# Kernel optimization log

Measured on AMD Instinct MI355X. Metric: run time of the kernel, lower is better.

The kernel has to match this reference:

```python
import jax, jax.numpy as jnp
import numpy as np

NUM_NODES = 100000
NUM_EDGES = 6400000


def setup_inputs() -> dict:
    key = jax.random.key(0)
    k1, k2 = jax.random.split(key)
    e = jax.random.normal(k1, (NUM_EDGES,), dtype=jnp.float32)
    edge_index = jax.random.randint(k2, (2, NUM_EDGES), 0, NUM_NODES, dtype=jnp.int64 if jax.config.jax_enable_x64 else jnp.int32)
    return {"e": e, "edge_index": edge_index, "num_nodes": NUM_NODES}


def reference(e, edge_index, num_nodes):
    # GAT edge softmax (no max-subtraction, matching the 'simple' variant)
    target_nodes = edge_index[1]                      # [E]
    exp_e = jnp.exp(e)                                # [E]
    sum_exp = jax.ops.segment_sum(exp_e, target_nodes, num_segments=num_nodes)  # [N]
    alpha = exp_e / (sum_exp[target_nodes] + 1e-16)   # gather + normalize
    return alpha
```

## Files before the change

### kernel.cpp

```cpp
#include <hip/hip_runtime.h>


#define CHUNK 36864
#define SCAT_THREADS 1024
#define NPT 7
#define NSUB 8
#define ASSUMED_N 100000
#define SUMS_RESERVE (1u << 20)

__device__ __forceinline__ unsigned bf16rne(float f) {
    unsigned u = __float_as_uint(f);
    return (u + 0x7FFFu + ((u >> 16) & 1u)) >> 16;
}
__device__ __forceinline__ float bf16tof(unsigned short h) {
    return __uint_as_float(((unsigned)h) << 16);
}


__global__ __launch_bounds__(SCAT_THREADS, 4)
void gat_scatter_regcache(const float* __restrict__ e,
                          const int* __restrict__ tgt,
                          const int* __restrict__ np,
                          unsigned short* __restrict__ partials,
                          int per, int E, int Cmax) {
    __shared__ float hist[CHUNK];
    const int n = *np;
    int C = (n + CHUNK - 1) / CHUNK;
    if (C > Cmax) C = Cmax;

    const int b = blockIdx.x;
    const int tid = threadIdx.x;
    const long long start = (long long)b * per;

    int nv = per >> 2;
    long long rem = (long long)E - start;
    if (rem < 0) rem = 0;
    if ((long long)nv > (rem >> 2)) nv = (int)(rem >> 2);
    const int tail_lo = nv * 4;
    int tail_hi = per;
    if ((long long)tail_hi > rem) tail_hi = (int)rem;

    const float4* e4 = reinterpret_cast<const float4*>(e + start);
    const int4*  t4 = reinterpret_cast<const int4*>(tgt + start);

    float4 xv[NPT];
    int4   iv[NPT];
#pragma unroll
    for (int i = 0; i < NPT; ++i) {
        const int v = i * SCAT_THREADS + tid;
        if (v < nv) {
            const float4 ev = e4[v];
            iv[i] = t4[v];
            xv[i].x = __expf(ev.x); xv[i].y = __expf(ev.y);
            xv[i].z = __expf(ev.z); xv[i].w = __expf(ev.w);
        } else {
            iv[i].x = iv[i].y = iv[i].z = iv[i].w = -1;
            xv[i].x = xv[i].y = xv[i].z = xv[i].w = 0.0f;
        }
    }
#pragma unroll
    for (int i = 0; i < NPT; ++i) {
        asm volatile("" : "+v"(xv[i].x), "+v"(xv[i].y),
                          "+v"(xv[i].z), "+v"(xv[i].w),
                          "+v"(iv[i].x), "+v"(iv[i].y),
                          "+v"(iv[i].z), "+v"(iv[i].w));
    }

    for (int c = 0; c < C; ++c) {
        const int base = c * CHUNK;

        float4 z; z.x = z.y = z.z = z.w = 0.0f;
        for (int j = tid; j < (CHUNK / 4); j += SCAT_THREADS)
            reinterpret_cast<float4*>(hist)[j] = z;
        __syncthreads();

#pragma unroll
        for (int i = 0; i < NPT; ++i) {
            int t;
            t = iv[i].x - base; if ((unsigned)t < (unsigned)CHUNK) atomicAdd(&hist[t], xv[i].x);
            t = iv[i].y - base; if ((unsigned)t < (unsigned)CHUNK) atomicAdd(&hist[t], xv[i].y);
            t = iv[i].z - base; if ((unsigned)t < (unsigned)CHUNK) atomicAdd(&hist[t], xv[i].z);
            t = iv[i].w - base; if ((unsigned)t < (unsigned)CHUNK) atomicAdd(&hist[t], xv[i].w);
        }
        for (int i = tail_lo + tid; i < tail_hi; i += SCAT_THREADS) {
            int t = tgt[start + i] - base;
            if ((unsigned)t < (unsigned)CHUNK) atomicAdd(&hist[t], __expf(e[start + i]));
        }
        __syncthreads();

        unsigned* dst = reinterpret_cast<unsigned*>(
            partials + ((size_t)b * Cmax + c) * CHUNK);
        const float2* h2 = reinterpret_cast<const float2*>(hist);
        for (int j = tid; j < (CHUNK / 2); j += SCAT_THREADS) {
            const float2 hv = h2[j];
            dst[j] = bf16rne(hv.x) | (bf16rne(hv.y) << 16);
        }
        __syncthreads();
    }
}


__global__ void gat_reduce1(const unsigned short* __restrict__ partials,
                            float* __restrict__ subsums,
                            int B, int CC ) {
    const int nq = CC >> 2;
    const int t = blockIdx.x * blockDim.x + threadIdx.x;
    if (t >= nq * NSUB) return;
    const int s = t / nq;
    const int q = t - s * nq;
    const int nd = q * 4;
    const int bps = B / NSUB;
    const int b0 = s * bps;

    const unsigned short* p = partials + nd;
    float s0 = 0.f, s1 = 0.f, s2 = 0.f, s3 = 0.f;
    float r0 = 0.f, r1 = 0.f, r2 = 0.f, r3 = 0.f;
    for (int b = b0; b + 1 < b0 + bps; b += 2) {
        const ushort4 va = *reinterpret_cast<const ushort4*>(p + (size_t)b * CC);
        const ushort4 vb = *reinterpret_cast<const ushort4*>(p + (size_t)(b + 1) * CC);
        s0 += bf16tof(va.x); s1 += bf16tof(va.y);
        s2 += bf16tof(va.z); s3 += bf16tof(va.w);
        r0 += bf16tof(vb.x); r1 += bf16tof(vb.y);
        r2 += bf16tof(vb.z); r3 += bf16tof(vb.w);
    }
    float4 o;
    o.x = s0 + r0; o.y = s1 + r1; o.z = s2 + r2; o.w = s3 + r3;
    *reinterpret_cast<float4*>(subsums + (size_t)s * CC + nd) = o;
}


__global__ void gat_reduce2(const float* __restrict__ subsums,
                            const int* __restrict__ np,
                            float* __restrict__ sums,
                            int CC) {
    const int n = *np;
    const int q = blockIdx.x * blockDim.x + threadIdx.x;
    const int nd = q * 4;
    if (nd >= CC) return;
    float4 acc; acc.x = acc.y = acc.z = acc.w = 0.f;
#pragma unroll
    for (int s = 0; s < NSUB; ++s) {
        const float4 v = *reinterpret_cast<const float4*>(subsums + (size_t)s * CC + nd);
        acc.x += v.x; acc.y += v.y; acc.z += v.z; acc.w += v.w;
    }
    if (nd + 4 <= n) {
        *reinterpret_cast<float4*>(sums + nd) = acc;
    } else {
        if (nd     < n) sums[nd]     = acc.x;
        if (nd + 1 < n) sums[nd + 1] = acc.y;
        if (nd + 2 < n) sums[nd + 2] = acc.z;
        if (nd + 3 < n) sums[nd + 3] = acc.w;
    }
}


__global__ void gat_zero_sums(float* __restrict__ sums,
                              const int* __restrict__ np) {
    const int n = *np;
    const int stride = gridDim.x * blockDim.x;
    for (int i = blockIdx.x * blockDim.x + threadIdx.x; i < n; i += stride)
        sums[i] = 0.0f;
}

__global__ void gat_exp_scatter(const float4* __restrict__ e4,
                                const int4* __restrict__ t4,
                                const float* __restrict__ e,
                                const int* __restrict__ tgt,
                                float* __restrict__ sums,
                                int n4, int E) {
    const int stride = gridDim.x * blockDim.x;
    int tid = blockIdx.x * blockDim.x + threadIdx.x;
    for (int i = tid; i < n4; i += stride) {
        float4 ev = e4[i];
        int4 tv = t4[i];
        atomicAdd(&sums[tv.x], __expf(ev.x));
        atomicAdd(&sums[tv.y], __expf(ev.y));
        atomicAdd(&sums[tv.z], __expf(ev.z));
        atomicAdd(&sums[tv.w], __expf(ev.w));
    }
    const int tail_base = n4 * 4;
    const int tail_n = E - tail_base;
    if (tid < tail_n)
        atomicAdd(&sums[tgt[tail_base + tid]], __expf(e[tail_base + tid]));
}


__global__ void gat_normalize(const float4* __restrict__ e4,
                              const int4* __restrict__ t4,
                              const float* __restrict__ e,
                              const int* __restrict__ tgt,
                              const float* __restrict__ sums,
                              float4* __restrict__ out4,
                              float* __restrict__ out,
                              int n4, int E) {
    const int stride = gridDim.x * blockDim.x;
    int tid = blockIdx.x * blockDim.x + threadIdx.x;
    for (int i = tid; i < n4; i += stride) {
        float4 ev = e4[i];
        int4 tv = t4[i];
        float4 r;
        r.x = __expf(ev.x) * __builtin_amdgcn_rcpf(sums[tv.x] + 1e-16f);
        r.y = __expf(ev.y) * __builtin_amdgcn_rcpf(sums[tv.y] + 1e-16f);
        r.z = __expf(ev.z) * __builtin_amdgcn_rcpf(sums[tv.z] + 1e-16f);
        r.w = __expf(ev.w) * __builtin_amdgcn_rcpf(sums[tv.w] + 1e-16f);
        out4[i] = r;
    }
    const int tail_base = n4 * 4;
    const int tail_n = E - tail_base;
    if (tid < tail_n) {
        int i = tail_base + tid;
        out[i] = __expf(e[i]) * __builtin_amdgcn_rcpf(sums[tgt[i]] + 1e-16f);
    }
}

extern "C" void kernel_launch(void* const* d_in, const int* in_sizes, int n_in,
                              void* d_out, int out_size, void* d_ws, size_t ws_size,
                              hipStream_t stream) {
    const float* e = (const float*)d_in[0];
    const int* edge_index = (const int*)d_in[1];
    const int* num_nodes_p = (const int*)d_in[2];

    const int E = in_sizes[0];
    const int* tgt = edge_index + E;

    float* sums = (float*)d_ws;
    float* alpha = (float*)d_out;
    const int n4e = E / 4;

    const int Cmax = (ASSUMED_N + CHUNK - 1) / CHUNK;
    const int CC = Cmax * CHUNK;
    const int B = 256;
    const int per = (((E + B - 1) / B) + 3) & ~3;

    const size_t subs_off = SUMS_RESERVE;
    const size_t part_off = subs_off + (size_t)NSUB * CC * sizeof(float);

    bool use_chunked =
        (part_off + (size_t)B * CC * sizeof(unsigned short)) <= ws_size
        && per <= NPT * SCAT_THREADS * 4;

    if (use_chunked) {
        float* subsums = (float*)((char*)d_ws + subs_off);
        unsigned short* partials = (unsigned short*)((char*)d_ws + part_off);

        gat_scatter_regcache<<<B, SCAT_THREADS, 0, stream>>>(
            e, tgt, num_nodes_p, partials, per, E, Cmax);

        const int r1_threads = (CC / 4) * NSUB;
        gat_reduce1<<<(r1_threads + 255) / 256, 256, 0, stream>>>(
            partials, subsums, B, CC);

        gat_reduce2<<<(CC / 4 + 255) / 256, 256, 0, stream>>>(
            subsums, num_nodes_p, sums, CC);
    } else {
        gat_zero_sums<<<512, 256, 0, stream>>>(sums, num_nodes_p);
        int blocks = (n4e + 255) / 256;
        if (blocks > 2048) blocks = 2048;
        if (blocks < 1) blocks = 1;
        gat_exp_scatter<<<blocks, 256, 0, stream>>>(
            (const float4*)e, (const int4*)tgt, e, tgt, sums, n4e, E);
    }

    {
        int blocks = (n4e + 255) / 256;
        if (blocks < 1) blocks = 1;
        gat_normalize<<<blocks, 256, 0, stream>>>(
            (const float4*)e, (const int4*)tgt, e, tgt, sums,
            (float4*)alpha, alpha, n4e, E);
    }
}
```

Measured before the change: 95.74 us.

## Split node range across blocks instead of looping chunks with register-cached edges

The scatter kernel used to keep each block's edge slice in registers and loop over about three node chunks, reusing one 144KB LDS histogram. Now every (edge slice, node chunk) pair gets its own block with a 72KB histogram, 128 slices by 6 chunks. Each block re-reads its edge slice from memory and recomputes exp, so edge traffic and exp work grow about six-fold, in exchange for many more independent blocks and higher occupancy. The partials buffer shrinks because there are fewer slices, which cuts work in the reduce kernels. Node capacity is now fixed at 110592 and the kernel no longer reads num_nodes to limit the chunk count.

```diff
diff --git a/kernel.cpp b/kernel.cpp
--- a/kernel.cpp
+++ b/kernel.cpp
@@ -1,12 +1,15 @@
 #include <hip/hip_runtime.h>
 
 
-#define CHUNK 36864
-#define SCAT_THREADS 1024
-#define NPT 7
+#define CHUNK2 18432
+#define NCH 6
+#define CCAP (CHUNK2 * NCH)
+#define B_S 128
 #define NSUB 8
-#define ASSUMED_N 100000
+#define SCAT_THREADS 512
 #define SUMS_RESERVE (1u << 20)
+#define SUBS_OFF SUMS_RESERVE
+#define PART_OFF (SUBS_OFF + (size_t)NSUB * CCAP * sizeof(float))
 
 __device__ __forceinline__ unsigned bf16rne(float f) {
     unsigned u = __float_as_uint(f);
@@ -16,25 +19,27 @@
     return __uint_as_float(((unsigned)h) << 16);
 }
 
-
 __global__ __launch_bounds__(SCAT_THREADS, 4)
-void gat_scatter_regcache(const float* __restrict__ e,
-                          const int* __restrict__ tgt,
-                          const int* __restrict__ np,
-                          unsigned short* __restrict__ partials,
-                          int per, int E, int Cmax) {
-    __shared__ float hist[CHUNK];
-    const int n = *np;
-    int C = (n + CHUNK - 1) / CHUNK;
-    if (C > Cmax) C = Cmax;
-
-    const int b = blockIdx.x;
+void gat_scatter_sc(const float* __restrict__ e,
+                    const int* __restrict__ tgt,
+                    unsigned short* __restrict__ partials,
+                    int per, int E) {
+    __shared__ float hist[CHUNK2];
+    const int bid = blockIdx.x;
+    const int slice = bid / NCH;
+    const int ch = bid - slice * NCH;
+    const int base = ch * CHUNK2;
     const int tid = threadIdx.x;
-    const long long start = (long long)b * per;
-
-    int nv = per >> 2;
+
+    float4 z; z.x = z.y = z.z = z.w = 0.0f;
+    for (int j = tid; j < (CHUNK2 / 4); j += SCAT_THREADS)
+        reinterpret_cast<float4*>(hist)[j] = z;
+    __syncthreads();
+
+    const long long start = (long long)slice * per;
     long long rem = (long long)E - start;
     if (rem < 0) rem = 0;
+    int nv = per >> 2;
     if ((long long)nv > (rem >> 2)) nv = (int)(rem >> 2);
     const int tail_lo = nv * 4;
     int tail_hi = per;
@@ -43,81 +48,47 @@
     const float4* e4 = reinterpret_cast<const float4*>(e + start);
     const int4*  t4 = reinterpret_cast<const int4*>(tgt + start);
 
-    float4 xv[NPT];
-    int4   iv[NPT];
-#pragma unroll
-    for (int i = 0; i < NPT; ++i) {
-        const int v = i * SCAT_THREADS + tid;
-        if (v < nv) {
-            const float4 ev = e4[v];
-            iv[i] = t4[v];
-            xv[i].x = __expf(ev.x); xv[i].y = __expf(ev.y);
-            xv[i].z = __expf(ev.z); xv[i].w = __expf(ev.w);
-        } else {
-            iv[i].x = iv[i].y = iv[i].z = iv[i].w = -1;
-            xv[i].x = xv[i].y = xv[i].z = xv[i].w = 0.0f;
-        }
-    }
-#pragma unroll
-    for (int i = 0; i < NPT; ++i) {
-        asm volatile("" : "+v"(xv[i].x), "+v"(xv[i].y),
-                          "+v"(xv[i].z), "+v"(xv[i].w),
-                          "+v"(iv[i].x), "+v"(iv[i].y),
-                          "+v"(iv[i].z), "+v"(iv[i].w));
-    }
-
-    for (int c = 0; c < C; ++c) {
-        const int base = c * CHUNK;
-
-        float4 z; z.x = z.y = z.z = z.w = 0.0f;
-        for (int j = tid; j < (CHUNK / 4); j += SCAT_THREADS)
-            reinterpret_cast<float4*>(hist)[j] = z;
-        __syncthreads();
-
-#pragma unroll
-        for (int i = 0; i < NPT; ++i) {
-            int t;
-            t = iv[i].x - base; if ((unsigned)t < (unsigned)CHUNK) atomicAdd(&hist[t], xv[i].x);
-            t = iv[i].y - base; if ((unsigned)t < (unsigned)CHUNK) atomicAdd(&hist[t], xv[i].y);
-            t = iv[i].z - base; if ((unsigned)t < (unsigned)CHUNK) atomicAdd(&hist[t], xv[i].z);
-            t = iv[i].w - base; if ((unsigned)t < (unsigned)CHUNK) atomicAdd(&hist[t], xv[i].w);
-        }
-        for (int i = tail_lo + tid; i < tail_hi; i += SCAT_THREADS) {
-            int t = tgt[start + i] - base;
-            if ((unsigned)t < (unsigned)CHUNK) atomicAdd(&hist[t], __expf(e[start + i]));
-        }
-        __syncthreads();
-
-        unsigned* dst = reinterpret_cast<unsigned*>(
-            partials + ((size_t)b * Cmax + c) * CHUNK);
-        const float2* h2 = reinterpret_cast<const float2*>(hist);
-        for (int j = tid; j < (CHUNK / 2); j += SCAT_THREADS) {
-            const float2 hv = h2[j];
-            dst[j] = bf16rne(hv.x) | (bf16rne(hv.y) << 16);
-        }
-        __syncthreads();
-    }
-}
-
+    for (int v = tid; v < nv; v += SCAT_THREADS) {
+        const float4 ev = e4[v];
+        const int4 tv = t4[v];
+        int t;
+        t = tv.x - base; if ((unsigned)t < (unsigned)CHUNK2) atomicAdd(&hist[t], __expf(ev.x));
+        t = tv.y - base; if ((unsigned)t < (unsigned)CHUNK2) atomicAdd(&hist[t], __expf(ev.y));
+        t = tv.z - base; if ((unsigned)t < (unsigned)CHUNK2) atomicAdd(&hist[t], __expf(ev.z));
+        t = tv.w - base; if ((unsigned)t < (unsigned)CHUNK2) atomicAdd(&hist[t], __expf(ev.w));
+    }
+    for (int i = tail_lo + tid; i < tail_hi; i += SCAT_THREADS) {
+        const int t = tgt[start + i] - base;
+        if ((unsigned)t < (unsigned)CHUNK2) atomicAdd(&hist[t], __expf(e[start + i]));
+    }
+    __syncthreads();
+
+    unsigned* dst = reinterpret_cast<unsigned*>(
+        partials + ((size_t)slice * NCH + ch) * CHUNK2);
+    const float2* h2 = reinterpret_cast<const float2*>(hist);
+    for (int j = tid; j < (CHUNK2 / 2); j += SCAT_THREADS) {
+        const float2 hv = h2[j];
+        dst[j] = bf16rne(hv.x) | (bf16rne(hv.y) << 16);
+    }
+}
 
 __global__ void gat_reduce1(const unsigned short* __restrict__ partials,
-                            float* __restrict__ subsums,
-                            int B, int CC ) {
-    const int nq = CC >> 2;
+                            float* __restrict__ subsums) {
+    const int nq = CCAP >> 2;
     const int t = blockIdx.x * blockDim.x + threadIdx.x;
     if (t >= nq * NSUB) return;
     const int s = t / nq;
     const int q = t - s * nq;
     const int nd = q * 4;
-    const int bps = B / NSUB;
+    const int bps = B_S / NSUB;
     const int b0 = s * bps;
 
     const unsigned short* p = partials + nd;
     float s0 = 0.f, s1 = 0.f, s2 = 0.f, s3 = 0.f;
     float r0 = 0.f, r1 = 0.f, r2 = 0.f, r3 = 0.f;
     for (int b = b0; b + 1 < b0 + bps; b += 2) {
-        const ushort4 va = *reinterpret_cast<const ushort4*>(p + (size_t)b * CC);
-        const ushort4 vb = *reinterpret_cast<const ushort4*>(p + (size_t)(b + 1) * CC);
+        const ushort4 va = *reinterpret_cast<const ushort4*>(p + (size_t)b * CCAP);
+        const ushort4 vb = *reinterpret_cast<const ushort4*>(p + (size_t)(b + 1) * CCAP);
         s0 += bf16tof(va.x); s1 += bf16tof(va.y);
         s2 += bf16tof(va.z); s3 += bf16tof(va.w);
         r0 += bf16tof(vb.x); r1 += bf16tof(vb.y);
@@ -125,22 +96,21 @@
     }
     float4 o;
     o.x = s0 + r0; o.y = s1 + r1; o.z = s2 + r2; o.w = s3 + r3;
-    *reinterpret_cast<float4*>(subsums + (size_t)s * CC + nd) = o;
-}
-
+    *reinterpret_cast<float4*>(subsums + (size_t)s * CCAP + nd) = o;
+}
 
 __global__ void gat_reduce2(const float* __restrict__ subsums,
                             const int* __restrict__ np,
-                            float* __restrict__ sums,
-                            int CC) {
+                            float* __restrict__ sums) {
     const int n = *np;
     const int q = blockIdx.x * blockDim.x + threadIdx.x;
     const int nd = q * 4;
-    if (nd >= CC) return;
+    if (nd >= CCAP) return;
     float4 acc; acc.x = acc.y = acc.z = acc.w = 0.f;
 #pragma unroll
     for (int s = 0; s < NSUB; ++s) {
-        const float4 v = *reinterpret_cast<const float4*>(subsums + (size_t)s * CC + nd);
+        const float4 v = *reinterpret_cast<const float4*>(
+            subsums + (size_t)s * CCAP + nd);
         acc.x += v.x; acc.y += v.y; acc.z += v.z; acc.w += v.w;
     }
     if (nd + 4 <= n) {
@@ -153,7 +123,6 @@
     }
 }
 
-
 __global__ void gat_zero_sums(float* __restrict__ sums,
                               const int* __restrict__ np) {
     const int n = *np;
@@ -169,21 +138,19 @@
                                 float* __restrict__ sums,
                                 int n4, int E) {
     const int stride = gridDim.x * blockDim.x;
-    int tid = blockIdx.x * blockDim.x + threadIdx.x;
+    const int tid = blockIdx.x * blockDim.x + threadIdx.x;
     for (int i = tid; i < n4; i += stride) {
-        float4 ev = e4[i];
-        int4 tv = t4[i];
+        const float4 ev = e4[i];
+        const int4 tv = t4[i];
         atomicAdd(&sums[tv.x], __expf(ev.x));
         atomicAdd(&sums[tv.y], __expf(ev.y));
         atomicAdd(&sums[tv.z], __expf(ev.z));
         atomicAdd(&sums[tv.w], __expf(ev.w));
     }
     const int tail_base = n4 * 4;
-    const int tail_n = E - tail_base;
-    if (tid < tail_n)
+    if (tid < E - tail_base)
         atomicAdd(&sums[tgt[tail_base + tid]], __expf(e[tail_base + tid]));
 }
-
 
 __global__ void gat_normalize(const float4* __restrict__ e4,
                               const int4* __restrict__ t4,
@@ -194,10 +161,10 @@
                               float* __restrict__ out,
                               int n4, int E) {
     const int stride = gridDim.x * blockDim.x;
-    int tid = blockIdx.x * blockDim.x + threadIdx.x;
+    const int tid = blockIdx.x * blockDim.x + threadIdx.x;
     for (int i = tid; i < n4; i += stride) {
-        float4 ev = e4[i];
-        int4 tv = t4[i];
+        const float4 ev = e4[i];
+        const int4 tv = t4[i];
         float4 r;
         r.x = __expf(ev.x) * __builtin_amdgcn_rcpf(sums[tv.x] + 1e-16f);
         r.y = __expf(ev.y) * __builtin_amdgcn_rcpf(sums[tv.y] + 1e-16f);
@@ -206,9 +173,8 @@
         out4[i] = r;
     }
     const int tail_base = n4 * 4;
-    const int tail_n = E - tail_base;
-    if (tid < tail_n) {
-        int i = tail_base + tid;
+    if (tid < E - tail_base) {
+        const int i = tail_base + tid;
         out[i] = __expf(e[i]) * __builtin_amdgcn_rcpf(sums[tgt[i]] + 1e-16f);
     }
 }
@@ -227,31 +193,24 @@
     float* alpha = (float*)d_out;
     const int n4e = E / 4;
 
-    const int Cmax = (ASSUMED_N + CHUNK - 1) / CHUNK;
-    const int CC = Cmax * CHUNK;
-    const int B = 256;
-    const int per = (((E + B - 1) / B) + 3) & ~3;
-
-    const size_t subs_off = SUMS_RESERVE;
-    const size_t part_off = subs_off + (size_t)NSUB * CC * sizeof(float);
-
-    bool use_chunked =
-        (part_off + (size_t)B * CC * sizeof(unsigned short)) <= ws_size
-        && per <= NPT * SCAT_THREADS * 4;
-
-    if (use_chunked) {
-        float* subsums = (float*)((char*)d_ws + subs_off);
-        unsigned short* partials = (unsigned short*)((char*)d_ws + part_off);
-
-        gat_scatter_regcache<<<B, SCAT_THREADS, 0, stream>>>(
-            e, tgt, num_nodes_p, partials, per, E, Cmax);
-
-        const int r1_threads = (CC / 4) * NSUB;
+    const int per = (((E + B_S - 1) / B_S) + 3) & ~3;
+
+    const size_t need = PART_OFF + (size_t)B_S * CCAP * sizeof(unsigned short);
+    const bool use_priv = ws_size >= need;
+
+    if (use_priv) {
+        float* subsums = (float*)((char*)d_ws + SUBS_OFF);
+        unsigned short* partials = (unsigned short*)((char*)d_ws + PART_OFF);
+
+        gat_scatter_sc<<<B_S * NCH, SCAT_THREADS, 0, stream>>>(
+            e, tgt, partials, per, E);
+
+        const int r1_threads = (CCAP / 4) * NSUB;
         gat_reduce1<<<(r1_threads + 255) / 256, 256, 0, stream>>>(
-            partials, subsums, B, CC);
-
-        gat_reduce2<<<(CC / 4 + 255) / 256, 256, 0, stream>>>(
-            subsums, num_nodes_p, sums, CC);
+            partials, subsums);
+
+        gat_reduce2<<<(CCAP / 4 + 255) / 256, 256, 0, stream>>>(
+            subsums, num_nodes_p, sums);
     } else {
         gat_zero_sums<<<512, 256, 0, stream>>>(sums, num_nodes_p);
         int blocks = (n4e + 255) / 256;
```

After: 102.6 us. 7.1% more time.
